# Kernel optimization log

Hardware: AMD Instinct MI355X
Metric: run time of the kernel (lower is better)

The kernel has to match this reference:

```python
import jax, jax.numpy as jnp
import numpy as np

# dims
B, P, H, W = 4, 512, 32, 32
C2 = P // 2            # 256 per-branch channels
HEAD = 4
DH = C2 // HEAD        # 64 head dim
L = H * W              # 1024 tokens
DI = 2 * C2            # 512 mamba d_inner (expand=2)
N = 64                 # d_state
R = (C2 + 15) // 16    # 16 dt_rank
KC = 4                 # d_conv


def setup_inputs() -> dict:
    key = jax.random.key(0)
    ks = jax.random.split(key, 32)
    f32 = jnp.float32
    def nrm(k, shape, s=0.02):
        return jax.random.normal(k, shape, f32) * s
    inp = {}
    inp['x'] = jax.random.normal(ks[0], (B, P, H, W), f32)
    # GambaCell rel-pos + gate conv
    inp['rel_h_c'] = jax.random.normal(ks[1], (1, C2, 1, H), f32)
    inp['rel_w_c'] = jax.random.normal(ks[2], (1, C2, W, 1), f32)
    inp['gate_w'] = nrm(ks[3], (C2, C2, 3))
    inp['gate_b'] = jnp.zeros((C2,), f32)
    # Mamba params
    inp['W_in'] = nrm(ks[4], (2 * DI, C2))
    inp['conv_w'] = nrm(ks[5], (DI, KC), 0.2)
    inp['conv_b'] = jnp.zeros((DI,), f32)
    inp['W_x'] = nrm(ks[6], (R + 2 * N, DI))
    inp['W_dt'] = nrm(ks[7], (DI, R), 0.1)
    inp['b_dt'] = jnp.full((DI,), -4.0, f32)
    inp['A_log'] = jnp.broadcast_to(jnp.log(jnp.arange(1, N + 1, dtype=f32)), (DI, N)).copy()
    inp['D_p'] = jnp.ones((DI,), f32)
    inp['W_out'] = nrm(ks[8], (C2, DI))
    # MHSA params (1x1 convs -> dense)
    inp['Wq'] = nrm(ks[9], (C2, C2)); inp['bq'] = jnp.zeros((C2,), f32)
    inp['Wk'] = nrm(ks[10], (C2, C2)); inp['bk'] = jnp.zeros((C2,), f32)
    inp['Wv'] = nrm(ks[11], (C2, C2)); inp['bv'] = jnp.zeros((C2,), f32)
    inp['rel_h_m'] = jax.random.normal(ks[12], (1, HEAD, DH, 1, H), f32) * 0.02
    inp['rel_w_m'] = jax.random.normal(ks[13], (1, HEAD, DH, W, 1), f32) * 0.02
    inp['reg_qk'] = jax.random.normal(ks[14], (1, L, L), f32)
    inp['reg_v'] = jax.random.normal(ks[15], (1, DH, L), f32)
    # Gating params
    inp['Wa'] = nrm(ks[16], (P, C2)); inp['ba'] = jnp.zeros((P,), f32)
    inp['Wb'] = nrm(ks[17], (P, C2)); inp['bb'] = jnp.zeros((P,), f32)
    inp['Wg'] = nrm(ks[18], (1, P)); inp['bg'] = jnp.zeros((1,), f32)
    return inp


def _silu(t):
    return t * jax.nn.sigmoid(t)


def _conv1x1(w, b, t):  # Conv2d kernel_size=1
    return jnp.einsum('oc,bchw->bohw', w, t) + b[None, :, None, None]


def _mamba(seq, W_in, conv_w, conv_b, W_x, W_dt, b_dt, A_log, D_p, W_out):
    # seq: (B, L, C2)
    Bn = seq.shape[0]
    xz = seq @ W_in.T                       # (B,L,2*DI)
    xi, z = jnp.split(xz, 2, axis=-1)
    # causal depthwise conv1d, kernel 4, left-pad 3, trimmed to L
    xc = jnp.transpose(xi, (0, 2, 1))       # (B,DI,L)
    xp = jnp.pad(xc, ((0, 0), (0, 0), (KC - 1, 0)))
    conv = conv_b[None, :, None]
    for kk in range(KC):
        conv = conv + conv_w[None, :, kk, None] * xp[:, :, kk:kk + L]
    xs = _silu(conv).transpose(0, 2, 1)     # (B,L,DI)
    x_dbl = xs @ W_x.T                      # (B,L,R+2N)
    dt = jax.nn.softplus(x_dbl[..., :R] @ W_dt.T + b_dt)   # (B,L,DI)
    Bm = x_dbl[..., R:R + N]                # (B,L,N)
    Cm = x_dbl[..., R + N:]                 # (B,L,N)
    A = -jnp.exp(A_log)                     # (DI,N)

    def step(h, t):
        dt_t, B_t, C_t, u_t = t             # (B,DI),(B,N),(B,N),(B,DI)
        dA = jnp.exp(dt_t[..., None] * A)   # (B,DI,N)
        h = dA * h + (dt_t * u_t)[..., None] * B_t[:, None, :]
        y = jnp.sum(h * C_t[:, None, :], axis=-1)
        return h, y

    h0 = jnp.zeros((Bn, DI, N), seq.dtype)
    scan_in = (dt.transpose(1, 0, 2), Bm.transpose(1, 0, 2),
               Cm.transpose(1, 0, 2), xs.transpose(1, 0, 2))
    _, ys = jax.lax.scan(step, h0, scan_in)  # (L,B,DI)
    y = ys.transpose(1, 0, 2) + D_p * xs
    y = y * _silu(z)
    return y @ W_out.T                      # (B,L,C2)


def _forward(x, rel_h_c, rel_w_c, gate_w, gate_b, W_in, conv_w, conv_b, W_x,
             W_dt, b_dt, A_log, D_p, W_out, Wq, bq, Wk, bk, Wv, bv,
             rel_h_m, rel_w_m, reg_qk, reg_v, Wa, ba, Wb, bb, Wg, bg):
    Bn = x.shape[0]
    x1, x2 = x[:, :C2], x[:, C2:]
    # --- GambaCell branch ---
    seq = x1.reshape(Bn, C2, L).transpose(0, 2, 1)          # (B,L,C2)
    pos = (rel_h_c + rel_w_c).reshape(1, C2, L).transpose(0, 2, 1)
    seq = seq + pos
    sc = seq.transpose(0, 2, 1)                             # (B,C2,L)
    ctx = jax.nn.sigmoid(
        jax.lax.conv_general_dilated(sc, gate_w, (1,), [(1, 1)],
                                     dimension_numbers=('NCH', 'OIH', 'NCH'))
        + gate_b[None, :, None]).transpose(0, 2, 1)          # (B,L,C2)
    ym = _mamba(seq, W_in, conv_w, conv_b, W_x, W_dt, b_dt, A_log, D_p, W_out)
    # faithful to original: view (B,L,C)->(B,C,H,W) with no permute
    out1 = (ym * ctx).reshape(Bn, C2, H, W)
    # --- MHSA branch ---
    q = _conv1x1(Wq, bq, x2).reshape(Bn, HEAD, DH, L)
    k = _conv1x1(Wk, bk, x2).reshape(Bn, HEAD, DH, L)
    v = _conv1x1(Wv, bv, x2).reshape(Bn, HEAD, DH, L)
    cc = jnp.einsum('bhdi,bhdj->bhij', q, k)                # content-content
    posm = (rel_h_m + rel_w_m).reshape(HEAD, DH, L)
    cp = jnp.einsum('hdi,bhdj->bhij', posm, q)              # position^T @ q
    energy = cc + cp                                         # (B,HEAD,L,L)
    e = jnp.concatenate([energy, jnp.broadcast_to(reg_qk[None], (Bn, 1, L, L))], axis=1)
    vp = jnp.concatenate([v, jnp.broadcast_to(reg_v[None], (Bn, 1, DH, L))], axis=1)
    attn = jax.nn.softmax(e, axis=-1)
    out = jnp.einsum('bndj,bnij->bndi', vp, attn)           # v @ attn^T
    out2 = out[:, :HEAD].reshape(Bn, C2, H, W)
    # --- Gating fusion ---
    a_proj = _conv1x1(Wa, ba, out1)
    b_proj = _conv1x1(Wb, bb, out2)
    ga = jax.nn.sigmoid(_conv1x1(Wg, bg, a_proj))
    gb = jax.nn.sigmoid(_conv1x1(Wg, bg, b_proj))
    return ga * a_proj + gb * b_proj                        # (B,P,H,W)


def reference(x, rel_h_c, rel_w_c, gate_w, gate_b, W_in, conv_w, conv_b, W_x,
              W_dt, b_dt, A_log, D_p, W_out, Wq, bq, Wk, bk, Wv, bv,
              rel_h_m, rel_w_m, reg_qk, reg_v, Wa, ba, Wb, bb, Wg, bg):
    return _forward(x, rel_h_c, rel_w_c, gate_w, gate_b, W_in, conv_w, conv_b,
                    W_x, W_dt, b_dt, A_log, D_p, W_out, Wq, bq, Wk, bk, Wv, bv,
                    rel_h_m, rel_w_m, reg_qk, reg_v, Wa, ba, Wb, bb, Wg, bg)
```

## Files before the change

### kernel.cpp

```cpp
#include <hip/hip_runtime.h>
#include <math.h>

static constexpr int Bn = 4, Pp = 512, C2 = 256, HEAD = 4, DHd = 64;
static constexpr int Ll = 1024, DIi = 512, Nn = 64, Rr = 16, KCc = 4;

#define DEVI __device__ __forceinline__

DEVI float sigf(float x){ return 1.0f/(1.0f+__expf(-x)); }
DEVI float softplusf(float x){ return x > 20.f ? x : log1pf(__expf(x)); }

DEVI unsigned short bfh(float f){
  unsigned int u = __float_as_uint(f);
  return (unsigned short)((u + 0x7FFFu + ((u>>16)&1u)) >> 16);
}
DEVI float bff(unsigned short h){ return __uint_as_float(((unsigned int)h)<<16); }

typedef __attribute__((ext_vector_type(8))) short  bf8v;
typedef __attribute__((ext_vector_type(4))) float  f4v;
typedef __attribute__((ext_vector_type(8))) unsigned short u16x8;

__global__ void k_transpose(const float* __restrict__ x, const float* __restrict__ rh,
                            const float* __restrict__ rw, float* __restrict__ seq,
                            float* __restrict__ x2seq){
  __shared__ float t[32][33];
  int b = blockIdx.z, c0 = blockIdx.y*32, l0 = blockIdx.x*32;
  for (int i = threadIdx.y; i < 32; i += 8)
    t[i][threadIdx.x] = x[((size_t)(b*Pp + c0 + i)*Ll) + l0 + threadIdx.x];
  __syncthreads();
  for (int i = threadIdx.y; i < 32; i += 8){
    int l = l0 + i, c = c0 + threadIdx.x;
    float v = t[threadIdx.x][i];
    if (c < C2){
      float pos = rh[c*32 + (l & 31)] + rw[c*32 + (l >> 5)];
      seq[(size_t)(b*Ll + l)*C2 + c] = v + pos;
    } else {
      x2seq[(size_t)(b*Ll + l)*C2 + (c - C2)] = v;
    }
  }
}

__global__ void __launch_bounds__(256) k_mgemmb(
    const float* __restrict__ A, const float* __restrict__ B,
    float* __restrict__ C, const float* __restrict__ bias,
    int M, int N, int K, int lda, int ldb, int ldc,
    long sA1, long sA2, long sB1, long sB2, long sC1, long sC2, int act)
{
  __shared__ __align__(16) unsigned short Ah[64*40], Al[64*40], Bh[64*40], Bl[64*40];
  int z = blockIdx.z;
  const float* Ab = A + (size_t)((z>>2)*sA1 + (z&3)*sA2);
  const float* Bb = B + (size_t)((z>>2)*sB1 + (z&3)*sB2);
  float*       Cb = C + (size_t)((z>>2)*sC1 + (z&3)*sC2);
  int m0 = blockIdx.y*64, n0 = blockIdx.x*64;
  int t = threadIdx.x;
  int w = t >> 6, l = t & 63;
  int g = l >> 4, r = l & 15;
  int row0 = w*16;

  f4v acc[4];
  #pragma unroll
  for (int j=0;j<4;++j) acc[j] = (f4v){0.f,0.f,0.f,0.f};

  int sr = t >> 2;
  int sc = (t & 3) * 8;

  for (int k0 = 0; k0 < K; k0 += 32){
    {
      const float* src = Ab + (size_t)(m0+sr)*lda + k0 + sc;
      float4 v0 = *(const float4*)(src);
      float4 v1 = *(const float4*)(src+4);
      float f[8] = {v0.x,v0.y,v0.z,v0.w,v1.x,v1.y,v1.z,v1.w};
      u16x8 hv, lv;
      #pragma unroll
      for (int i=0;i<8;++i){
        unsigned short h = bfh(f[i]); hv[i] = h;
        lv[i] = bfh(f[i] - bff(h));
      }
      *(u16x8*)&Ah[sr*40+sc] = hv;
      *(u16x8*)&Al[sr*40+sc] = lv;
    }
    {
      const float* src = Bb + (size_t)(n0+sr)*ldb + k0 + sc;
      float4 v0 = *(const float4*)(src);
      float4 v1 = *(const float4*)(src+4);
      float f[8] = {v0.x,v0.y,v0.z,v0.w,v1.x,v1.y,v1.z,v1.w};
      u16x8 hv, lv;
      #pragma unroll
      for (int i=0;i<8;++i){
        unsigned short h = bfh(f[i]); hv[i] = h;
        lv[i] = bfh(f[i] - bff(h));
      }
      *(u16x8*)&Bh[sr*40+sc] = hv;
      *(u16x8*)&Bl[sr*40+sc] = lv;
    }
    __syncthreads();
    bf8v a_h = *(const bf8v*)&Ah[(row0+r)*40 + g*8];
    bf8v a_l = *(const bf8v*)&Al[(row0+r)*40 + g*8];
    #pragma unroll
    for (int j=0;j<4;++j){
      bf8v b_h = *(const bf8v*)&Bh[(j*16+r)*40 + g*8];
      bf8v b_l = *(const bf8v*)&Bl[(j*16+r)*40 + g*8];
      acc[j] = __builtin_amdgcn_mfma_f32_16x16x32_bf16(a_h, b_h, acc[j], 0, 0, 0);
      acc[j] = __builtin_amdgcn_mfma_f32_16x16x32_bf16(a_h, b_l, acc[j], 0, 0, 0);
      acc[j] = __builtin_amdgcn_mfma_f32_16x16x32_bf16(a_l, b_h, acc[j], 0, 0, 0);
    }
    __syncthreads();
  }
  #pragma unroll
  for (int j=0;j<4;++j){
    int n = n0 + j*16 + r;
    float bv = bias ? bias[n] : 0.f;
    #pragma unroll
    for (int q=0;q<4;++q){
      int m = m0 + row0 + g*4 + q;
      float v = acc[j][q] + bv;
      if (act == 1) v = sigf(v);
      Cb[(size_t)m*ldc + n] = v;
    }
  }
}

__global__ void __launch_bounds__(256) k_gemm(
       const float* __restrict__ A, const float* __restrict__ B,
       float* __restrict__ C, const float* __restrict__ bias,
       int M, int N, int K, int lda, int ldb, int ldc, int act)
{
  __shared__ float As[16][64];
  __shared__ float Bs[16][64];
  int m0 = blockIdx.y*64, n0 = blockIdx.x*64;
  int t = threadIdx.x, tx = t & 15, ty = t >> 4;
  float acc[4][4] = {};
  int arow = t >> 2, akq = (t & 3) * 4;
  for (int k0 = 0; k0 < K; k0 += 16){
    float4 av = *(const float4*)(A + (size_t)(m0+arow)*lda + k0 + akq);
    As[akq+0][arow] = av.x; As[akq+1][arow] = av.y;
    As[akq+2][arow] = av.z; As[akq+3][arow] = av.w;
    float4 bv = make_float4(0.f,0.f,0.f,0.f);
    if (n0 + arow < N) bv = *(const float4*)(B + (size_t)(n0+arow)*ldb + k0 + akq);
    Bs[akq+0][arow]=bv.x; Bs[akq+1][arow]=bv.y;
    Bs[akq+2][arow]=bv.z; Bs[akq+3][arow]=bv.w;
    __syncthreads();
    #pragma unroll
    for (int k = 0; k < 16; ++k){
      float4 a = *(const float4*)&As[k][ty*4];
      float4 b = *(const float4*)&Bs[k][tx*4];
      acc[0][0] = fmaf(a.x,b.x,acc[0][0]); acc[0][1] = fmaf(a.x,b.y,acc[0][1]);
      acc[0][2] = fmaf(a.x,b.z,acc[0][2]); acc[0][3] = fmaf(a.x,b.w,acc[0][3]);
      acc[1][0] = fmaf(a.y,b.x,acc[1][0]); acc[1][1] = fmaf(a.y,b.y,acc[1][1]);
      acc[1][2] = fmaf(a.y,b.z,acc[1][2]); acc[1][3] = fmaf(a.y,b.w,acc[1][3]);
      acc[2][0] = fmaf(a.z,b.x,acc[2][0]); acc[2][1] = fmaf(a.z,b.y,acc[2][1]);
      acc[2][2] = fmaf(a.z,b.z,acc[2][2]); acc[2][3] = fmaf(a.z,b.w,acc[2][3]);
      acc[3][0] = fmaf(a.w,b.x,acc[3][0]); acc[3][1] = fmaf(a.w,b.y,acc[3][1]);
      acc[3][2] = fmaf(a.w,b.z,acc[3][2]); acc[3][3] = fmaf(a.w,b.w,acc[3][3]);
    }
    __syncthreads();
  }
  #pragma unroll
  for (int i = 0; i < 4; ++i){
    int m = m0 + ty*4 + i;
    #pragma unroll
    for (int j = 0; j < 4; ++j){
      int n = n0 + tx*4 + j;
      if (n < N){
        float v = acc[i][j];
        if (bias) v += bias[n];
        if (act == 1) v = sigf(v);
        else if (act == 2) v = softplusf(v);
        C[(size_t)m*ldc + n] = v;
      }
    }
  }
}

__global__ void k_im2col(const float* __restrict__ seq, float* __restrict__ A2){
  int idx = blockIdx.x*256 + threadIdx.x;
  int j  = idx % 768;
  int bl = idx / 768;
  int kk = j >> 8, c = j & 255;
  int l = bl & 1023, b = bl >> 10;
  int ls = l + kk - 1;
  float v = 0.f;
  if (ls >= 0 && ls < Ll) v = seq[(size_t)(b*Ll + ls)*C2 + c];
  A2[idx] = v;
}

__global__ void k_packw(const float* __restrict__ gw, float* __restrict__ W2){
  int idx = blockIdx.x*256 + threadIdx.x;
  int j = idx % 768, o = idx / 768;
  int kk = j >> 8, i = j & 255;
  W2[idx] = gw[(size_t)(o*256 + i)*3 + kk];
}

__global__ void k_dwconv(const float* __restrict__ xz, const float* __restrict__ cw,
                         const float* __restrict__ cb, float* __restrict__ xs){
  int idx = blockIdx.x*256 + threadIdx.x;
  int d = idx & 511; int bl = idx >> 9; int l = bl & 1023; int b = bl >> 10;
  float s = cb[d];
  #pragma unroll
  for (int kk = 0; kk < 4; ++kk){
    int ls = l - 3 + kk;
    if (ls >= 0) s = fmaf(cw[d*4+kk], xz[(size_t)(b*Ll+ls)*1024 + d], s);
  }
  xs[idx] = s * sigf(s);
}

__global__ void k_pret(const float* __restrict__ xdbl, const float* __restrict__ xs,
                       const float* __restrict__ W_dt, const float* __restrict__ b_dt,
                       float* __restrict__ dtT, float* __restrict__ dtuT){
  __shared__ float X[32][17];
  __shared__ float Wd[32][17];
  __shared__ float xsb[32][33];
  int b = blockIdx.z, d0 = blockIdx.y*32, l0 = blockIdx.x*32;
  int tx = threadIdx.x, ty = threadIdx.y;
  for (int i = ty; i < 32; i += 8){
    if (tx < 16)      X[i][tx]      = xdbl[(size_t)(b*Ll + l0 + i)*144 + tx];
    else              Wd[i][tx-16]  = W_dt[(size_t)(d0 + i)*16 + tx - 16];
    xsb[i][tx] = xs[(size_t)(b*Ll + l0 + i)*512 + d0 + tx];
  }
  __syncthreads();
  for (int dy = ty; dy < 32; dy += 8){
    int d = d0 + dy;
    float v = b_dt[d];
    #pragma unroll
    for (int r = 0; r < 16; ++r) v = fmaf(Wd[dy][r], X[tx][r], v);
    float dt = softplusf(v);
    size_t o = ((size_t)(b*512 + d))*Ll + l0 + tx;
    dtT[o]  = dt;
    dtuT[o] = dt * xsb[tx][dy];
  }
}

__global__ void __launch_bounds__(64) k_scan4(
    const float* __restrict__ dtT, const float* __restrict__ dtuT,
    const float* __restrict__ xdbl, const float* __restrict__ A_log,
    float* __restrict__ yT){
  __shared__ float Bs[32*64];
  __shared__ float Cs[32*64];
  __shared__ float pb[32*65];
  int lane = threadIdx.x;
  int wid  = blockIdx.x;
  int b = wid >> 9, d = wid & 511;
  float Ac = -__expf(A_log[d*64 + lane]);
  float h = 0.f;
  size_t base = (size_t)b*Ll;
  size_t bd   = (size_t)wid*Ll;
  int jl = lane & 31;
  bool lo = lane < 32;
  for (int c0 = 0; c0 < Ll; c0 += 32){
    float dtv = 0.f, duv = 0.f;
    if (lo){
      dtv = dtT[bd + c0 + lane];
      duv = dtuT[bd + c0 + lane];
    }
    for (int l = 0; l < 32; ++l){
      size_t r2 = (base + c0 + l)*144;
      Bs[l*64 + lane] = xdbl[r2 + 16 + lane];
      Cs[l*64 + lane] = xdbl[r2 + 80 + lane];
    }
    __syncthreads();
    #pragma unroll
    for (int l = 0; l < 32; ++l){
      float sdt = __shfl(dtv, l);
      float sdu = __shfl(duv, l);
      float dA = __expf(sdt*Ac);
      h = fmaf(dA, h, sdu*Bs[l*64 + lane]);
      pb[l*65 + lane] = h*Cs[l*64 + lane];
    }
    __syncthreads();
    {
      const float* rp = &pb[jl*65 + (lo ? 0 : 32)];
      float s0=0.f, s1=0.f, s2=0.f, s3=0.f;
      #pragma unroll
      for (int n = 0; n < 32; n += 4){
        s0 += rp[n]; s1 += rp[n+1]; s2 += rp[n+2]; s3 += rp[n+3];
      }
      float p = (s0+s1)+(s2+s3);
      p += __shfl_xor(p, 32);
      if (lo) yT[bd + c0 + jl] = p;
    }
    __syncthreads();
  }
}

__global__ void k_ytrans(const float* __restrict__ yT, const float* __restrict__ xs,
                         const float* __restrict__ xz, const float* __restrict__ D_p,
                         float* __restrict__ y){
  __shared__ float t[32][33];
  int b = blockIdx.z, d0 = blockIdx.y*32, l0 = blockIdx.x*32;
  int tx = threadIdx.x, ty = threadIdx.y;
  for (int i = ty; i < 32; i += 8)
    t[i][tx] = yT[((size_t)(b*512 + d0 + i))*Ll + l0 + tx];
  __syncthreads();
  for (int i = ty; i < 32; i += 8){
    int d = d0 + tx;
    size_t bl = (size_t)b*Ll + l0 + i;
    float p  = t[tx][i];
    float u  = xs[bl*512 + d];
    float zv = xz[bl*1024 + 512 + d];
    y[bl*512 + d] = (p + D_p[d]*u) * (zv * sigf(zv));
  }
}

__global__ void k_pack_ab(const float* __restrict__ qt, const float* __restrict__ kt,
                          const float* __restrict__ rhm, const float* __restrict__ rwm,
                          float* __restrict__ Ab, float* __restrict__ Bb){
  int idx = blockIdx.x*256 + threadIdx.x;
  int dd = idx & 127;
  int i  = (idx >> 7) & 1023;
  int h  = (idx >> 17) & 3;
  int b  = idx >> 19;
  float av, bv;
  if (dd < 64){
    size_t q = (size_t)(b*Ll + i)*C2 + h*64 + dd;
    av = qt[q]; bv = kt[q];
  } else {
    int d = dd - 64;
    av = rhm[(h*64+d)*32 + (i & 31)] + rwm[(h*64+d)*32 + (i >> 5)];
    bv = qt[(size_t)(b*Ll + i)*C2 + h*64 + d];
  }
  Ab[idx] = av; Bb[idx] = bv;
}

__global__ void k_vtrans(const float* __restrict__ vt, float* __restrict__ vT){
  __shared__ float t[32][33];
  int b = blockIdx.z, c0 = blockIdx.y*32, j0 = blockIdx.x*32;
  for (int i = threadIdx.y; i < 32; i += 8)
    t[i][threadIdx.x] = vt[(size_t)(b*Ll + j0 + i)*C2 + c0 + threadIdx.x];
  __syncthreads();
  for (int i = threadIdx.y; i < 32; i += 8)
    vT[((size_t)(b*C2 + c0 + i))*Ll + j0 + threadIdx.x] = t[threadIdx.x][i];
}

__global__ void __launch_bounds__(256) k_softmax(float* __restrict__ e){
  __shared__ float red[4];
  __shared__ float red2[4];
  size_t row = blockIdx.x;
  float* p = e + row*1024;
  int t = threadIdx.x;
  float v0 = p[t], v1 = p[t+256], v2 = p[t+512], v3 = p[t+768];
  float mx = fmaxf(fmaxf(v0,v1), fmaxf(v2,v3));
  #pragma unroll
  for (int off=32; off; off>>=1) mx = fmaxf(mx, __shfl_xor(mx, off));
  if ((t&63)==0) red[t>>6] = mx;
  __syncthreads();
  mx = fmaxf(fmaxf(red[0],red[1]), fmaxf(red[2],red[3]));
  v0 = __expf(v0-mx); v1 = __expf(v1-mx); v2 = __expf(v2-mx); v3 = __expf(v3-mx);
  float s = v0+v1+v2+v3;
  #pragma unroll
  for (int off=32; off; off>>=1) s += __shfl_xor(s, off);
  if ((t&63)==0) red2[t>>6] = s;
  __syncthreads();
  s = red2[0]+red2[1]+red2[2]+red2[3];
  float inv = 1.0f/s;
  p[t] = v0*inv; p[t+256] = v1*inv; p[t+512] = v2*inv; p[t+768] = v3*inv;
}

__global__ void k_mulshuf(const float* __restrict__ ym, const float* __restrict__ ctx,
                          float* __restrict__ out1t){
  __shared__ float t[32][33];
  int b = blockIdx.z >> 2, s1 = blockIdx.z & 3;
  int c0 = blockIdx.y*32, s00 = blockIdx.x*32;
  for (int i = threadIdx.y; i < 32; i += 8){
    int c = c0 + i;
    int l = c*4 + s1;
    size_t off = ((size_t)(b*Ll + l))*C2 + s00 + threadIdx.x;
    t[i][threadIdx.x] = ym[off] * ctx[off];
  }
  __syncthreads();
  for (int i = threadIdx.y; i < 32; i += 8){
    int s0 = s00 + i, c = c0 + threadIdx.x;
    int s = s1*256 + s0;
    out1t[((size_t)(b*Ll + s))*C2 + c] = t[threadIdx.x][i];
  }
}

__global__ void __launch_bounds__(256) k_gates(
    const float* __restrict__ ap, const float* __restrict__ bp,
    const float* __restrict__ Wg, const float* __restrict__ bg, float* __restrict__ g){
  __shared__ float ra[4], rb[4];
  int bl = blockIdx.x; int t = threadIdx.x;
  float sa = 0.f, sb = 0.f;
  const float* a = ap + (size_t)bl*512;
  const float* bq = bp + (size_t)bl*512;
  for (int pp = t; pp < 512; pp += 256){ float w = Wg[pp]; sa = fmaf(w, a[pp], sa); sb = fmaf(w, bq[pp], sb); }
  #pragma unroll
  for (int off=32; off; off>>=1){ sa += __shfl_xor(sa,off); sb += __shfl_xor(sb,off); }
  if ((t&63)==0){ ra[t>>6]=sa; rb[t>>6]=sb; }
  __syncthreads();
  if (t==0){
    float b0 = bg[0];
    g[bl]        = sigf(ra[0]+ra[1]+ra[2]+ra[3] + b0);
    g[4096 + bl] = sigf(rb[0]+rb[1]+rb[2]+rb[3] + b0);
  }
}

__global__ void k_final(const float* __restrict__ ap, const float* __restrict__ bp,
                        const float* __restrict__ g, float* __restrict__ out){
  int bpid = blockIdx.x; int b = bpid >> 9, p = bpid & 511;
  for (int l = threadIdx.x; l < Ll; l += 256){
    int bl = b*Ll + l;
    float ga = g[bl], gb = g[4096 + bl];
    out[((size_t)(b*Pp + p) << 10) + l] =
        ga*ap[(size_t)bl*512 + p] + gb*bp[(size_t)bl*512 + p];
  }
}

static inline void mgemm(hipStream_t s, const float* A, const float* B, float* C,
                         const float* bias, int M, int N, int K, int lda, int ldb, int ldc,
                         int act){
  dim3 g(N/64, M/64, 1), blk(256);
  k_mgemmb<<<g, blk, 0, s>>>(A,B,C,bias,M,N,K,lda,ldb,ldc, 0,0,0,0,0,0, act);
}

extern "C" void kernel_launch(void* const* d_in, const int* in_sizes, int n_in,
                              void* d_out, int out_size, void* d_ws, size_t ws_size,
                              hipStream_t stream) {
  const float* x      = (const float*)d_in[0];
  const float* rh_c   = (const float*)d_in[1];
  const float* rw_c   = (const float*)d_in[2];
  const float* gate_w = (const float*)d_in[3];
  const float* gate_b = (const float*)d_in[4];
  const float* W_in   = (const float*)d_in[5];
  const float* conv_w = (const float*)d_in[6];
  const float* conv_b = (const float*)d_in[7];
  const float* W_x    = (const float*)d_in[8];
  const float* W_dt   = (const float*)d_in[9];
  const float* b_dt   = (const float*)d_in[10];
  const float* A_log  = (const float*)d_in[11];
  const float* D_p    = (const float*)d_in[12];
  const float* W_out  = (const float*)d_in[13];
  const float* Wq     = (const float*)d_in[14];
  const float* bq     = (const float*)d_in[15];
  const float* Wk     = (const float*)d_in[16];
  const float* bk     = (const float*)d_in[17];
  const float* Wv     = (const float*)d_in[18];
  const float* bv     = (const float*)d_in[19];
  const float* rhm    = (const float*)d_in[20];
  const float* rwm    = (const float*)d_in[21];
  const float* Wa     = (const float*)d_in[24];
  const float* ba     = (const float*)d_in[25];
  const float* Wb     = (const float*)d_in[26];
  const float* bb     = (const float*)d_in[27];
  const float* Wg     = (const float*)d_in[28];
  const float* bg     = (const float*)d_in[29];
  float* out = (float*)d_out;
  float* ws  = (float*)d_ws;

  float* seq    = ws;
  float* x2seq  = ws +  1048576;
  float* qt     = ws +  2097152;
  float* kt     = ws +  3145728;
  float* vt     = ws +  4194304;
  float* Abuf   = ws +  5242880;
  float* Bbuf   = ws +  7340032;
  float* arena  = ws +  9437184;
  float* out2   = ws + 26214400;
  float* out1   = ws + 27262976;
  float* aproj  = ws + 28311552;
  float* bproj  = ws + 30408704;
  float* gates  = ws + 32505856;
  float* W2     = ws + 32514048;
  float* A2   = arena;
  float* ctx  = arena +  3145728;
  float* xz   = arena +  4194304;
  float* xs   = arena +  8388608;
  float* xdbl = arena + 10485760;
  float* yT   = arena + 11075584;
  float* yb   = arena + 13172736;
  float* ym   = arena + 15269888;
  float* energy = arena;
  float* vT   = aproj;
  float* dtT  = Abuf;
  float* dtuT = Bbuf;

  k_transpose<<<dim3(32,16,4), dim3(32,8), 0, stream>>>(x, rh_c, rw_c, seq, x2seq);

  mgemm(stream, x2seq, Wq, qt, bq, 4096,256,256, 256,256,256, 0);
  mgemm(stream, x2seq, Wk, kt, bk, 4096,256,256, 256,256,256, 0);
  mgemm(stream, x2seq, Wv, vt, bv, 4096,256,256, 256,256,256, 0);
  k_pack_ab<<<8192, 256, 0, stream>>>(qt, kt, rhm, rwm, Abuf, Bbuf);
  k_vtrans<<<dim3(32,8,4), dim3(32,8), 0, stream>>>(vt, vT);
  {
    dim3 g(16, 16, 16), blk(256);
    k_mgemmb<<<g, blk, 0, stream>>>(Abuf, Bbuf, energy, nullptr,
        1024,1024,128, 128,128,1024,
        4L*131072, 131072, 4L*131072, 131072, 4L*1048576, 1048576, 0);
  }
  k_softmax<<<16384, 256, 0, stream>>>(energy);
  {
    dim3 g(1, 16, 16), blk(256);
    k_mgemmb<<<g, blk, 0, stream>>>(energy, vT, out2, nullptr,
        1024,64,1024, 1024,1024,256,
        4L*1048576, 1048576, 262144, 65536, 262144, 64, 0);
  }

  k_packw<<<768, 256, 0, stream>>>(gate_w, W2);
  k_im2col<<<12288, 256, 0, stream>>>(seq, A2);
  mgemm(stream, A2, W2, ctx, gate_b, 4096,256,768, 768,768,256, 1);
  mgemm(stream, seq, W_in, xz, nullptr, 4096,1024,256, 256,256,1024, 0);
  k_dwconv<<<8192, 256, 0, stream>>>(xz, conv_w, conv_b, xs);
  {
    dim3 g(3, 64, 1), blk(256);
    k_gemm<<<g, blk, 0, stream>>>(xs, W_x, xdbl, nullptr, 4096,144,512, 512,512,144, 0);
  }
  k_pret<<<dim3(32,16,4), dim3(32,8), 0, stream>>>(xdbl, xs, W_dt, b_dt, dtT, dtuT);
  k_scan4<<<2048, 64, 0, stream>>>(dtT, dtuT, xdbl, A_log, yT);
  k_ytrans<<<dim3(32,16,4), dim3(32,8), 0, stream>>>(yT, xs, xz, D_p, yb);
  mgemm(stream, yb, W_out, ym, nullptr, 4096,256,512, 512,512,256, 0);
  k_mulshuf<<<dim3(8,8,16), dim3(32,8), 0, stream>>>(ym, ctx, out1);

  mgemm(stream, out1, Wa, aproj, ba, 4096,512,256, 256,256,512, 0);
  mgemm(stream, out2, Wb, bproj, bb, 4096,512,256, 256,256,512, 0);
  k_gates<<<4096, 256, 0, stream>>>(aproj, bproj, Wg, bg, gates);
  k_final<<<2048, 256, 0, stream>>>(aproj, bproj, gates, out);
}
```

Measured before the change: 645.2 us.

## Use 128x128 split-bf16 MFMA GEMM tiles and share scan B/C loads across channels

Adds a 128x128-tile split-bf16 MFMA GEMM kernel and uses it for the attention energy GEMM and the Mamba input projection. Larger tiles mean fewer blocks and more operand reuse per load. The selective-scan kernel now packs four channels per 256-thread block, so the per-timestep B/C state rows are staged in shared memory once and reused by four channels instead of being reloaded per channel. The cost is more registers, more LDS per block and fewer blocks in flight, which may lower occupancy.

```diff
diff --git a/kernel.cpp b/kernel.cpp
--- a/kernel.cpp
+++ b/kernel.cpp
@@ -115,6 +115,112 @@
       float v = acc[j][q] + bv;
       if (act == 1) v = sigf(v);
       Cb[(size_t)m*ldc + n] = v;
+    }
+  }
+}
+
+__global__ void __launch_bounds__(256) k_m128(
+    const float* __restrict__ A, const float* __restrict__ B,
+    float* __restrict__ C, const float* __restrict__ bias,
+    int M, int N, int K, int lda, int ldb, int ldc,
+    long sA1, long sA2, long sB1, long sB2, long sC1, long sC2, int act)
+{
+  __shared__ __align__(16) unsigned short Ah[128*40], Al[128*40], Bh[128*40], Bl[128*40];
+  int z = blockIdx.z;
+  const float* Ab = A + (size_t)((z>>2)*sA1 + (z&3)*sA2);
+  const float* Bb = B + (size_t)((z>>2)*sB1 + (z&3)*sB2);
+  float*       Cb = C + (size_t)((z>>2)*sC1 + (z&3)*sC2);
+  int m0 = blockIdx.y*128, n0 = blockIdx.x*128;
+  int t = threadIdx.x;
+  int w = t >> 6, l = t & 63;
+  int g = l >> 4, r = l & 15;
+  int row0 = w*32;
+
+  f4v acc[2][8];
+  #pragma unroll
+  for (int i=0;i<2;++i)
+    #pragma unroll
+    for (int j=0;j<8;++j) acc[i][j] = (f4v){0.f,0.f,0.f,0.f};
+
+  int sr = t >> 1;
+  int sc = (t & 1) * 16;
+
+  for (int k0 = 0; k0 < K; k0 += 32){
+    {
+      const float* src = Ab + (size_t)(m0+sr)*lda + k0 + sc;
+      float4 v0 = *(const float4*)(src);
+      float4 v1 = *(const float4*)(src+4);
+      float4 v2 = *(const float4*)(src+8);
+      float4 v3 = *(const float4*)(src+12);
+      float f[16] = {v0.x,v0.y,v0.z,v0.w,v1.x,v1.y,v1.z,v1.w,
+                     v2.x,v2.y,v2.z,v2.w,v3.x,v3.y,v3.z,v3.w};
+      u16x8 hv0, lv0, hv1, lv1;
+      #pragma unroll
+      for (int i=0;i<8;++i){
+        unsigned short h = bfh(f[i]); hv0[i] = h;
+        lv0[i] = bfh(f[i] - bff(h));
+      }
+      #pragma unroll
+      for (int i=0;i<8;++i){
+        unsigned short h = bfh(f[8+i]); hv1[i] = h;
+        lv1[i] = bfh(f[8+i] - bff(h));
+      }
+      *(u16x8*)&Ah[sr*40+sc]   = hv0;  *(u16x8*)&Ah[sr*40+sc+8] = hv1;
+      *(u16x8*)&Al[sr*40+sc]   = lv0;  *(u16x8*)&Al[sr*40+sc+8] = lv1;
+    }
+    {
+      const float* src = Bb + (size_t)(n0+sr)*ldb + k0 + sc;
+      float4 v0 = *(const float4*)(src);
+      float4 v1 = *(const float4*)(src+4);
+      float4 v2 = *(const float4*)(src+8);
+      float4 v3 = *(const float4*)(src+12);
+      float f[16] = {v0.x,v0.y,v0.z,v0.w,v1.x,v1.y,v1.z,v1.w,
+                     v2.x,v2.y,v2.z,v2.w,v3.x,v3.y,v3.z,v3.w};
+      u16x8 hv0, lv0, hv1, lv1;
+      #pragma unroll
+      for (int i=0;i<8;++i){
+        unsigned short h = bfh(f[i]); hv0[i] = h;
+        lv0[i] = bfh(f[i] - bff(h));
+      }
+      #pragma unroll
+      for (int i=0;i<8;++i){
+        unsigned short h = bfh(f[8+i]); hv1[i] = h;
+        lv1[i] = bfh(f[8+i] - bff(h));
+      }
+      *(u16x8*)&Bh[sr*40+sc]   = hv0;  *(u16x8*)&Bh[sr*40+sc+8] = hv1;
+      *(u16x8*)&Bl[sr*40+sc]   = lv0;  *(u16x8*)&Bl[sr*40+sc+8] = lv1;
+    }
+    __syncthreads();
+    bf8v a_h0 = *(const bf8v*)&Ah[(row0+r)*40 + g*8];
+    bf8v a_l0 = *(const bf8v*)&Al[(row0+r)*40 + g*8];
+    bf8v a_h1 = *(const bf8v*)&Ah[(row0+16+r)*40 + g*8];
+    bf8v a_l1 = *(const bf8v*)&Al[(row0+16+r)*40 + g*8];
+    #pragma unroll
+    for (int j=0;j<8;++j){
+      bf8v b_h = *(const bf8v*)&Bh[(j*16+r)*40 + g*8];
+      bf8v b_l = *(const bf8v*)&Bl[(j*16+r)*40 + g*8];
+      acc[0][j] = __builtin_amdgcn_mfma_f32_16x16x32_bf16(a_h0, b_h, acc[0][j], 0, 0, 0);
+      acc[0][j] = __builtin_amdgcn_mfma_f32_16x16x32_bf16(a_h0, b_l, acc[0][j], 0, 0, 0);
+      acc[0][j] = __builtin_amdgcn_mfma_f32_16x16x32_bf16(a_l0, b_h, acc[0][j], 0, 0, 0);
+      acc[1][j] = __builtin_amdgcn_mfma_f32_16x16x32_bf16(a_h1, b_h, acc[1][j], 0, 0, 0);
+      acc[1][j] = __builtin_amdgcn_mfma_f32_16x16x32_bf16(a_h1, b_l, acc[1][j], 0, 0, 0);
+      acc[1][j] = __builtin_amdgcn_mfma_f32_16x16x32_bf16(a_l1, b_h, acc[1][j], 0, 0, 0);
+    }
+    __syncthreads();
+  }
+  #pragma unroll
+  for (int i=0;i<2;++i){
+    #pragma unroll
+    for (int j=0;j<8;++j){
+      int n = n0 + j*16 + r;
+      float bv = bias ? bias[n] : 0.f;
+      #pragma unroll
+      for (int q=0;q<4;++q){
+        int m = m0 + row0 + i*16 + g*4 + q;
+        float v = acc[i][j][q] + bv;
+        if (act == 1) v = sigf(v);
+        Cb[(size_t)m*ldc + n] = v;
+      }
     }
   }
 }
@@ -229,32 +335,38 @@
   }
 }
 
-__global__ void __launch_bounds__(64) k_scan4(
+__global__ void __launch_bounds__(256) k_scan5(
     const float* __restrict__ dtT, const float* __restrict__ dtuT,
     const float* __restrict__ xdbl, const float* __restrict__ A_log,
     float* __restrict__ yT){
   __shared__ float Bs[32*64];
   __shared__ float Cs[32*64];
-  __shared__ float pb[32*65];
-  int lane = threadIdx.x;
-  int wid  = blockIdx.x;
-  int b = wid >> 9, d = wid & 511;
+  __shared__ float pb[4*32*65];
+  int t = threadIdx.x;
+  int w = t >> 6, lane = t & 63;
+  int blk = blockIdx.x;
+  int b = blk >> 7, grp = blk & 127;
+  int d = grp*4 + w;
   float Ac = -__expf(A_log[d*64 + lane]);
   float h = 0.f;
   size_t base = (size_t)b*Ll;
-  size_t bd   = (size_t)wid*Ll;
+  size_t bd   = ((size_t)(b*512 + d))*Ll;
   int jl = lane & 31;
   bool lo = lane < 32;
+  float* pbw = &pb[w*2080];
   for (int c0 = 0; c0 < Ll; c0 += 32){
     float dtv = 0.f, duv = 0.f;
     if (lo){
       dtv = dtT[bd + c0 + lane];
       duv = dtuT[bd + c0 + lane];
     }
-    for (int l = 0; l < 32; ++l){
-      size_t r2 = (base + c0 + l)*144;
-      Bs[l*64 + lane] = xdbl[r2 + 16 + lane];
-      Cs[l*64 + lane] = xdbl[r2 + 80 + lane];
+    #pragma unroll
+    for (int kk = 0; kk < 8; ++kk){
+      int i = t + kk*256;
+      int row = i >> 6, col = i & 63;
+      size_t r2 = (base + c0 + row)*144;
+      Bs[i] = xdbl[r2 + 16 + col];
+      Cs[i] = xdbl[r2 + 80 + col];
     }
     __syncthreads();
     #pragma unroll
@@ -263,11 +375,11 @@
       float sdu = __shfl(duv, l);
       float dA = __expf(sdt*Ac);
       h = fmaf(dA, h, sdu*Bs[l*64 + lane]);
-      pb[l*65 + lane] = h*Cs[l*64 + lane];
+      pbw[l*65 + lane] = h*Cs[l*64 + lane];
     }
     __syncthreads();
     {
-      const float* rp = &pb[jl*65 + (lo ? 0 : 32)];
+      const float* rp = &pbw[jl*65 + (lo ? 0 : 32)];
       float s0=0.f, s1=0.f, s2=0.f, s3=0.f;
       #pragma unroll
       for (int n = 0; n < 32; n += 4){
@@ -480,8 +592,8 @@
   k_pack_ab<<<8192, 256, 0, stream>>>(qt, kt, rhm, rwm, Abuf, Bbuf);
   k_vtrans<<<dim3(32,8,4), dim3(32,8), 0, stream>>>(vt, vT);
   {
-    dim3 g(16, 16, 16), blk(256);
-    k_mgemmb<<<g, blk, 0, stream>>>(Abuf, Bbuf, energy, nullptr,
+    dim3 g(8, 8, 16), blk(256);
+    k_m128<<<g, blk, 0, stream>>>(Abuf, Bbuf, energy, nullptr,
         1024,1024,128, 128,128,1024,
         4L*131072, 131072, 4L*131072, 131072, 4L*1048576, 1048576, 0);
   }
@@ -496,14 +608,18 @@
   k_packw<<<768, 256, 0, stream>>>(gate_w, W2);
   k_im2col<<<12288, 256, 0, stream>>>(seq, A2);
   mgemm(stream, A2, W2, ctx, gate_b, 4096,256,768, 768,768,256, 1);
-  mgemm(stream, seq, W_in, xz, nullptr, 4096,1024,256, 256,256,1024, 0);
+  {
+    dim3 g(8, 32, 1), blk(256);
+    k_m128<<<g, blk, 0, stream>>>(seq, W_in, xz, nullptr,
+        4096,1024,256, 256,256,1024, 0,0,0,0,0,0, 0);
+  }
   k_dwconv<<<8192, 256, 0, stream>>>(xz, conv_w, conv_b, xs);
   {
     dim3 g(3, 64, 1), blk(256);
     k_gemm<<<g, blk, 0, stream>>>(xs, W_x, xdbl, nullptr, 4096,144,512, 512,512,144, 0);
   }
   k_pret<<<dim3(32,16,4), dim3(32,8), 0, stream>>>(xdbl, xs, W_dt, b_dt, dtT, dtuT);
-  k_scan4<<<2048, 64, 0, stream>>>(dtT, dtuT, xdbl, A_log, yT);
+  k_scan5<<<512, 256, 0, stream>>>(dtT, dtuT, xdbl, A_log, yT);
   k_ytrans<<<dim3(32,16,4), dim3(32,8), 0, stream>>>(yT, xs, xz, D_p, yb);
   mgemm(stream, yb, W_out, ym, nullptr, 4096,256,512, 512,512,256, 0);
   k_mulshuf<<<dim3(8,8,16), dim3(32,8), 0, stream>>>(ym, ctx, out1);
```

Measured after the change: 575.4 us. 1.12x faster.
